# Kernel optimization log

Hardware: AMD Instinct MI355X
Metric: run time of the kernel (lower is better)

## Reference

```python
import jax, jax.numpy as jnp
import numpy as np

N, D, H, DH, FF, NE, NNZ = 4096, 128, 2, 64, 256, 2048, 65536
EPS = 1e-5

def layer_norm(x, g, b):
    m = jnp.mean(x, axis=-1, keepdims=True)
    v = jnp.var(x, axis=-1, keepdims=True)
    return (x - m) / jnp.sqrt(v + EPS) * g + b

def setup_inputs() -> dict:
    key = jax.random.key(0)
    ks = jax.random.split(key, 24)
    s = 0.05
    node_idx = jax.random.randint(ks[1], (NNZ,), 0, N)
    he_idx = jax.random.randint(ks[2], (NNZ,), 0, NE)
    return {
        "x": jax.random.normal(ks[0], (N, D), dtype=jnp.float32),
        "edge": jnp.stack([node_idx, he_idx]).astype(jnp.int64),
        "Wq": jax.random.normal(ks[3], (D, D)) * s, "bq": jnp.zeros((D,)),
        "Wk": jax.random.normal(ks[4], (D, D)) * s, "bk": jnp.zeros((D,)),
        "Wv": jax.random.normal(ks[5], (D, D)) * s, "bv": jnp.zeros((D,)),
        "Wo": jax.random.normal(ks[6], (D, D)) * s, "bo": jnp.zeros((D,)),
        "g_ln1": jnp.ones((D,)), "b_ln1": jnp.zeros((D,)),
        "W1": jax.random.normal(ks[7], (D, FF)) * s, "bf1": jnp.zeros((FF,)),
        "W2": jax.random.normal(ks[8], (FF, D)) * s, "bf2": jnp.zeros((D,)),
        "g_ln2": jnp.ones((D,)), "b_ln2": jnp.zeros((D,)),
        "Wh": jax.random.normal(ks[9], (D, D)) * s, "bh": jnp.zeros((D,)),
    }

def reference(x, edge, Wq, bq, Wk, bk, Wv, bv, Wo, bo, g_ln1, b_ln1,
              W1, bf1, W2, bf2, g_ln2, b_ln2, Wh, bh):
    # dropout layers run in eval mode (identity) for a deterministic reference
    def mha_block(h):
        q = (h @ Wq + bq).reshape(N, H, DH)
        k = (h @ Wk + bk).reshape(N, H, DH)
        v = (h @ Wv + bv).reshape(N, H, DH)
        scores = jnp.einsum('nhd,mhd->hnm', q, k) / jnp.sqrt(jnp.float32(DH))
        attn = jax.nn.softmax(scores, axis=-1)            # [H,N,N]
        o = jnp.einsum('hnm,mhd->nhd', attn, v).reshape(N, D)
        return layer_norm(h + o @ Wo + bo, g_ln1, b_ln1)

    def ff_block(h):
        z = jax.nn.sigmoid(h @ W1 + bf1)
        return layer_norm(h + z @ W2 + bf2, g_ln2, b_ln2)

    h = ff_block(mha_block(x))
    h = ff_block(mha_block(h))

    # HypergraphConv: out = D^{-1} H B^{-1} H^T (X Theta) + bias
    node_idx = edge[0]
    he_idx = edge[1]
    xt = h @ Wh                                            # [N,D]
    ones = jnp.ones((NNZ,), dtype=xt.dtype)
    Bdeg = jax.ops.segment_sum(ones, he_idx, num_segments=NE)
    Binv = jnp.where(Bdeg > 0, 1.0 / Bdeg, 0.0)
    Ddeg = jax.ops.segment_sum(ones, node_idx, num_segments=N)
    Dinv = jnp.where(Ddeg > 0, 1.0 / Ddeg, 0.0)
    e = jax.ops.segment_sum(xt[node_idx], he_idx, num_segments=NE) * Binv[:, None]
    out = jax.ops.segment_sum(e[he_idx], node_idx, num_segments=N) * Dinv[:, None] + bh
    return jax.nn.relu(out)
```

## Files before the change

kernel.cpp:

```cpp
#include <hip/hip_runtime.h>
#include <hip/hip_bf16.h>
#include <cstddef>

#define N_NODES 4096
#define DIM     128
#define NHEAD   2
#define DHEAD   64
#define FFDIM   256
#define NEDGE   2048
#define NNZ_E   65536
#define NSPLIT  8

typedef __attribute__((ext_vector_type(8))) short bf16x8;
typedef __attribute__((ext_vector_type(4))) float f32x4;
typedef unsigned short u16;

__device__ __forceinline__ u16 f2b(float f) {
    unsigned u = __float_as_uint(f);
    return (u16)((u + 0x7FFFu + ((u >> 16) & 1u)) >> 16);
}
__device__ __forceinline__ float b2f_bits(u16 h) {
    return __uint_as_float(((unsigned)h) << 16);
}
__device__ __forceinline__ unsigned cvtpk(float a, float b) {
    unsigned r;
    asm("v_cvt_pk_bf16_f32 %0, %1, %2" : "=v"(r) : "v"(a), "v"(b));
    return r;
}

__global__ void prep(const float* __restrict__ x, float* __restrict__ h,
                     u16* __restrict__ hh, u16* __restrict__ hl,
                     const float* W0, const float* W1, const float* W2,
                     const float* W3, const float* W4, const float* W5,
                     const float* W6,
                     u16* P0, u16* P1, u16* P2, u16* P3, u16* P4, u16* P5, u16* P6,
                     const int* __restrict__ edge_raw,
                     int* __restrict__ nidx, int* __restrict__ hidx,
                     int* __restrict__ cnt_e, int* __restrict__ cnt_n) {
    const int bx = blockIdx.x;
    if (bx < 512) {
        int i4 = bx * 256 + threadIdx.x;
        float4 f4 = ((const float4*)x)[i4];
        ((float4*)h)[i4] = f4;
        ushort4 hi4, lo4;
        hi4.x = f2b(f4.x); lo4.x = f2b(f4.x - b2f_bits(hi4.x));
        hi4.y = f2b(f4.y); lo4.y = f2b(f4.y - b2f_bits(hi4.y));
        hi4.z = f2b(f4.z); lo4.z = f2b(f4.z - b2f_bits(hi4.z));
        hi4.w = f2b(f4.w); lo4.w = f2b(f4.w - b2f_bits(hi4.w));
        ((ushort4*)hh)[i4] = hi4;
        ((ushort4*)hl)[i4] = lo4;
        return;
    }
    if (bx >= 1408) {
        __shared__ int is64_s;
        if (threadIdx.x < 64) {
            int v = edge_raw[2 * threadIdx.x + 1];
            unsigned long long bal = __ballot(v != 0);
            if (threadIdx.x == 0) is64_s = (bal == 0ull) ? 1 : 0;
        }
        __syncthreads();
        const int is64 = is64_s;
        int i = (bx - 1408) * 256 + threadIdx.x;
        if (i < NNZ_E) {
            int ni = (is64 ? edge_raw[2 * i]             : edge_raw[i])         & (N_NODES - 1);
            int he = (is64 ? edge_raw[2 * NNZ_E + 2 * i] : edge_raw[NNZ_E + i]) & (NEDGE - 1);
            nidx[i] = ni;
            hidx[i] = he;
            atomicAdd(&cnt_n[ni], 1);
            atomicAdd(&cnt_e[he], 1);
        }
        return;
    }
    const int p = bx - 512;
    const int sel = p >> 7;
    const float* W; u16* P; int K, NC;
    switch (sel) {
        case 0: W = W0; P = P0; K = 128; NC = 128; break;
        case 1: W = W1; P = P1; K = 128; NC = 128; break;
        case 2: W = W2; P = P2; K = 128; NC = 128; break;
        case 3: W = W3; P = P3; K = 128; NC = 128; break;
        case 4: W = W4; P = P4; K = 128; NC = 128; break;
        case 5: W = W5; P = P5; K = 128; NC = 256; break;
        default: W = W6; P = P6; K = 256; NC = 128; break;
    }
    int i = (p & 127) * 256 + threadIdx.x;
    if (i < K * NC) {
        int k = i / NC, n = i % NC;
        float f = W[i];
        u16 hb = f2b(f);
        size_t o = ((size_t)(k >> 3) * NC + n) * 8 + (k & 7);
        P[o] = hb;
        P[(size_t)K * NC + o] = f2b(f - b2f_bits(hb));
    }
}

__global__ __launch_bounds__(256) void qkv_mfma(const u16* __restrict__ Ah,
                                                const u16* __restrict__ Al,
                                                const u16* __restrict__ Wq,
                                                const u16* __restrict__ Wk,
                                                const u16* __restrict__ Wv,
                                                const float* __restrict__ bq,
                                                const float* __restrict__ bk,
                                                const float* __restrict__ bv,
                                                u16* __restrict__ qb,
                                                u16* __restrict__ kb,
                                                u16* __restrict__ vtb) {
    const int K = 128, NC = 128;
    const int tid = threadIdx.x, w = tid >> 6, lane = tid & 63;
    const int qi = lane & 15, gi = lane >> 4;
    const int row0 = blockIdx.x * 64 + w * 16;
    const int sel = blockIdx.y >> 2;
    const int col0 = (blockIdx.y & 3) * 32;
    const u16* Wp = (sel == 0) ? Wq : (sel == 1) ? Wk : Wv;
    const float* bias = (sel == 0) ? bq : (sel == 1) ? bk : bv;
    const u16* Wlo = Wp + (size_t)K * NC;

    f32x4 acc[2];
    acc[0] = (f32x4){0.f, 0.f, 0.f, 0.f};
    acc[1] = (f32x4){0.f, 0.f, 0.f, 0.f};

#pragma unroll 4
    for (int kc = 0; kc < K / 32; ++kc) {
        const int k0 = kc * 32;
        const size_t ao = (size_t)(row0 + qi) * K + k0 + gi * 8;
        bf16x8 ah = *(const bf16x8*)(Ah + ao);
        bf16x8 al = *(const bf16x8*)(Al + ao);
#pragma unroll
        for (int c = 0; c < 2; ++c) {
            const size_t wo = ((size_t)(k0 / 8 + gi) * NC + col0 + c * 16 + qi) * 8;
            bf16x8 wh = *(const bf16x8*)(Wp + wo);
            bf16x8 wl = *(const bf16x8*)(Wlo + wo);
            acc[c] = __builtin_amdgcn_mfma_f32_16x16x32_bf16(ah, wh, acc[c], 0, 0, 0);
            acc[c] = __builtin_amdgcn_mfma_f32_16x16x32_bf16(al, wh, acc[c], 0, 0, 0);
            acc[c] = __builtin_amdgcn_mfma_f32_16x16x32_bf16(ah, wl, acc[c], 0, 0, 0);
        }
    }

#pragma unroll
    for (int c = 0; c < 2; ++c) {
        const int col = col0 + c * 16 + qi;
        const int hh = col >> 6, d = col & 63;
        float bv_ = bias[col];
        if (sel < 2) {
            u16* dst = (sel == 0) ? qb : kb;
#pragma unroll
            for (int r = 0; r < 4; ++r) {
                const int grow = row0 + gi * 4 + r;
                dst[((size_t)hh * N_NODES + grow) * 64 + d] = f2b(acc[c][r] + bv_);
            }
        } else {
            const int grow0 = row0 + gi * 4;
            uint2 pw;
            pw.x = cvtpk(acc[c][0] + bv_, acc[c][1] + bv_);
            pw.y = cvtpk(acc[c][2] + bv_, acc[c][3] + bv_);
            *(uint2*)&vtb[((size_t)hh * 64 + d) * N_NODES + grow0] = pw;
        }
    }
}

#define ROWP 72
__global__ __launch_bounds__(512, 4) void attn_mfma(const u16* __restrict__ qb,
                                                    const u16* __restrict__ kb,
                                                    const u16* __restrict__ vtb,
                                                    float* __restrict__ op,
                                                    float* __restrict__ mlm,
                                                    float* __restrict__ mll,
                                                    const int* __restrict__ cnt_e,
                                                    const int* __restrict__ cnt_n,
                                                    int* __restrict__ off_e,
                                                    int* __restrict__ off_n,
                                                    int* __restrict__ cur_e,
                                                    int* __restrict__ cur_n) {
    __shared__ __align__(16) u16 k_s[2][64 * ROWP];
    __shared__ __align__(16) u16 vt_s[2][64 * ROWP];
    __shared__ __align__(16) u16 p_s[8][16 * ROWP];

    if (blockIdx.x >= 32) {
        if (blockIdx.y == 0 && blockIdx.z < 2) {
            int* sbuf = (int*)&k_s[0][0];
            const int he_side = (blockIdx.z == 0);
            const int n = he_side ? NEDGE : N_NODES;
            const int* cnt = he_side ? cnt_e : cnt_n;
            int* off = he_side ? off_e : off_n;
            int* cur = he_side ? cur_e : cur_n;
            for (int i = threadIdx.x; i < n; i += 512) sbuf[i] = cnt[i];
            __syncthreads();
            for (int st = 1; st < n; st <<= 1) {
                int v[8]; int nj = 0;
                for (int i = threadIdx.x; i < n; i += 512) v[nj++] = (i >= st) ? sbuf[i - st] : 0;
                __syncthreads();
                nj = 0;
                for (int i = threadIdx.x; i < n; i += 512) sbuf[i] += v[nj++];
                __syncthreads();
            }
            for (int i = threadIdx.x; i < n; i += 512) { off[i + 1] = sbuf[i]; cur[i] = 0; }
            if (threadIdx.x == 0) off[0] = 0;
        }
        return;
    }

    const int h = blockIdx.y;
    const int s = blockIdx.z;
    const int row0 = blockIdx.x * 128;
    const int tid = threadIdx.x;
    const int w = tid >> 6, lane = tid & 63;
    const int qi = lane & 15, gi = lane >> 4;
    const float CE = 0.18033688011f;
    const float THR = 44.36f;

    const u16* qrow = qb + ((size_t)h * N_NODES + row0 + w * 16 + qi) * 64 + gi * 8;
    bf16x8 qf0 = *(const bf16x8*)qrow;
    bf16x8 qf1 = *(const bf16x8*)(qrow + 32);

    f32x4 oc[4];
#pragma unroll
    for (int i = 0; i < 4; ++i) oc[i] = (f32x4){0.f, 0.f, 0.f, 0.f};
    float m_run = -INFINITY, l_run = 0.f;

    const u16* kbh = kb + (size_t)h * N_NODES * 64;
    const u16* vth = vtb + (size_t)h * 64 * N_NODES;

    const int nt0 = s * (N_NODES / 64 / NSPLIT);
    const int nt1 = nt0 + N_NODES / 64 / NSPLIT;
    const int r = tid >> 3, ss = tid & 7;

    {
        const u16* ksrc = kbh + nt0 * 64 * 64;
        *(uint4*)&k_s[0][r * ROWP + ss * 8]  = *(const uint4*)(ksrc + tid * 8);
        *(uint4*)&vt_s[0][r * ROWP + ss * 8] = *(const uint4*)(vth + (size_t)r * N_NODES + nt0 * 64 + ss * 8);
    }
    __syncthreads();
    int cur = 0;

    for (int kt = nt0; kt < nt1; ++kt) {
        uint4 knx, vnx;
        const bool more = (kt + 1 < nt1);
        if (more) {
            const u16* ksrc = kbh + (kt + 1) * 64 * 64;
            knx = *(const uint4*)(ksrc + tid * 8);
            vnx = *(const uint4*)(vth + (size_t)r * N_NODES + (kt + 1) * 64 + ss * 8);
        }

        f32x4 sc[4];
        __builtin_amdgcn_s_setprio(1);
#pragma unroll
        for (int t = 0; t < 4; ++t) {
            const u16* krow = &k_s[cur][(t * 16 + qi) * ROWP + gi * 8];
            bf16x8 ka0 = *(const bf16x8*)krow;
            bf16x8 ka1 = *(const bf16x8*)(krow + 32);
            f32x4 z = (f32x4){0.f, 0.f, 0.f, 0.f};
            z = __builtin_amdgcn_mfma_f32_16x16x32_bf16(ka0, qf0, z, 0, 0, 0);
            sc[t] = __builtin_amdgcn_mfma_f32_16x16x32_bf16(ka1, qf1, z, 0, 0, 0);
        }
        __builtin_amdgcn_s_setprio(0);

        float smax = -INFINITY;
#pragma unroll
        for (int t = 0; t < 4; ++t)
            smax = fmaxf(smax, fmaxf(fmaxf(sc[t][0], sc[t][1]), fmaxf(sc[t][2], sc[t][3])));
        smax = fmaxf(smax, __shfl_xor(smax, 16));
        smax = fmaxf(smax, __shfl_xor(smax, 32));

        const bool renew = !__all(smax <= m_run + THR);
        float alpha;
        if (renew) {
            float mn = fmaxf(m_run, smax);
            alpha = exp2f((m_run - mn) * CE);
            m_run = mn;
        }
        float nb = m_run * CE;
        float psum = 0.f;
#pragma unroll
        for (int t = 0; t < 4; ++t) {
            float p0 = exp2f(fmaf(sc[t][0], CE, -nb));
            float p1 = exp2f(fmaf(sc[t][1], CE, -nb));
            float p2 = exp2f(fmaf(sc[t][2], CE, -nb));
            float p3 = exp2f(fmaf(sc[t][3], CE, -nb));
            psum += (p0 + p1) + (p2 + p3);
            uint2 pw;
            pw.x = cvtpk(p0, p1);
            pw.y = cvtpk(p2, p3);
            *(uint2*)&p_s[w][qi * ROWP + t * 16 + gi * 4] = pw;
        }
        psum += __shfl_xor(psum, 16);
        psum += __shfl_xor(psum, 32);

        if (renew) {
            float a0 = __shfl(alpha, gi * 4 + 0);
            float a1 = __shfl(alpha, gi * 4 + 1);
            float a2 = __shfl(alpha, gi * 4 + 2);
            float a3 = __shfl(alpha, gi * 4 + 3);
#pragma unroll
            for (int d = 0; d < 4; ++d) {
                oc[d][0] *= a0; oc[d][1] *= a1; oc[d][2] *= a2; oc[d][3] *= a3;
            }
            l_run = l_run * alpha + psum;
        } else {
            l_run += psum;
        }

        const u16* prow = &p_s[w][qi * ROWP];
        bf16x8 pa0 = *(const bf16x8*)(prow + gi * 8);
        bf16x8 pa1 = *(const bf16x8*)(prow + 32 + gi * 8);
        __builtin_amdgcn_s_setprio(1);
#pragma unroll
        for (int d = 0; d < 4; ++d) {
            const u16* vrow = &vt_s[cur][(d * 16 + qi) * ROWP + gi * 8];
            bf16x8 vb0 = *(const bf16x8*)vrow;
            bf16x8 vb1 = *(const bf16x8*)(vrow + 32);
            oc[d] = __builtin_amdgcn_mfma_f32_16x16x32_bf16(pa0, vb0, oc[d], 0, 0, 0);
            oc[d] = __builtin_amdgcn_mfma_f32_16x16x32_bf16(pa1, vb1, oc[d], 0, 0, 0);
        }
        __builtin_amdgcn_s_setprio(0);

        if (more) {
            *(uint4*)&k_s[cur ^ 1][r * ROWP + ss * 8]  = knx;
            *(uint4*)&vt_s[cur ^ 1][r * ROWP + ss * 8] = vnx;
        }
        __syncthreads();
        cur ^= 1;
    }

    float* opd = op + (size_t)s * N_NODES * 128;
#pragma unroll
    for (int d = 0; d < 4; ++d) {
        size_t cb = h * 64 + d * 16 + qi;
        opd[(size_t)(row0 + w * 16 + gi * 4 + 0) * 128 + cb] = oc[d][0];
        opd[(size_t)(row0 + w * 16 + gi * 4 + 1) * 128 + cb] = oc[d][1];
        opd[(size_t)(row0 + w * 16 + gi * 4 + 2) * 128 + cb] = oc[d][2];
        opd[(size_t)(row0 + w * 16 + gi * 4 + 3) * 128 + cb] = oc[d][3];
    }
    if (gi == 0) {
        size_t mi = (size_t)s * NHEAD * N_NODES + (size_t)h * N_NODES + row0 + w * 16 + qi;
        mlm[mi] = m_run;
        mll[mi] = l_run;
    }
}

#define ROWA 136
#define ROWZ 264
#define ROWH 132
template<int DO_QKV>
__global__ __launch_bounds__(512) void mega_layer(
        const float* __restrict__ op, const float* __restrict__ mlm,
        const float* __restrict__ mll,
        const u16* __restrict__ wp_o, const float* __restrict__ bo,
        float* __restrict__ h,
        const float* __restrict__ g1, const float* __restrict__ b1,
        const u16* __restrict__ wp_1, const float* __restrict__ bf1,
        const u16* __restrict__ wp_2, const float* __restrict__ bf2,
        const float* __restrict__ g2, const float* __restrict__ b2,
        const u16* __restrict__ wp_q, const u16* __restrict__ wp_k,
        const u16* __restrict__ wp_v,
        const float* __restrict__ bq, const float* __restrict__ bk,
        const float* __restrict__ bv,
        u16* __restrict__ qb, u16* __restrict__ kb, u16* __restrict__ vtb,
        const u16* __restrict__ wp_h, float* __restrict__ xt,
        const int* __restrict__ nidx, const int* __restrict__ hidx,
        const int* __restrict__ off_e, const int* __restrict__ off_n,
        int* __restrict__ cur_e, int* __restrict__ cur_n,
        int* __restrict__ csr_e, int* __restrict__ csr_n) {
    if (DO_QKV && blockIdx.x >= N_NODES / 16) {
        int i = (blockIdx.x - N_NODES / 16) * 512 + threadIdx.x;
        if (i < NNZ_E) {
            int ni = nidx[i], he = hidx[i];
            int p = atomicAdd(&cur_e[he], 1);
            csr_e[off_e[he] + p] = ni;
            int q = atomicAdd(&cur_n[ni], 1);
            csr_n[off_n[ni] + q] = he;
        }
        return;
    }
    __shared__ __align__(16) u16 zbuf[16 * ROWZ * 2];
    __shared__ __align__(16) u16 hp_hi[16 * ROWA];
    __shared__ __align__(16) u16 hp_lo[16 * ROWA];
    __shared__ float hln[16 * ROWH];
    __shared__ float ws_s[NSPLIT][32];
    __shared__ float Linv_s[32];
    __shared__ float wsum[8][16], wsq[8][16];
    const float CE = 0.18033688011f;
    const int tid = threadIdx.x, w = tid >> 6, lane = tid & 63;
    const int qi = lane & 15, gi = lane >> 4;
    const int row0 = blockIdx.x * 16;
    u16* a_hi = zbuf;
    u16* a_lo = zbuf + 16 * ROWA;
    u16* z_hi = zbuf;
    u16* z_lo = zbuf + 16 * ROWZ;

    if (tid < 32) {
        int r = tid >> 1, hd = tid & 1;
        size_t mb = (size_t)hd * N_NODES + row0 + r;
        float m[NSPLIT], l[NSPLIT], mx = -INFINITY;
#pragma unroll
        for (int s = 0; s < NSPLIT; ++s) {
            m[s] = mlm[mb + (size_t)s * NHEAD * N_NODES];
            l[s] = mll[mb + (size_t)s * NHEAD * N_NODES];
            mx = fmaxf(mx, m[s]);
        }
        float L = 0.f;
#pragma unroll
        for (int s = 0; s < NSPLIT; ++s) {
            float ws = exp2f((m[s] - mx) * CE);
            ws_s[s][tid] = ws;
            L += ws * l[s];
        }
        Linv_s[tid] = 1.f / L;
    }
    __syncthreads();

    for (int e = tid; e < 16 * 128; e += 512) {
        int r = e >> 7, c = e & 127, hd = c >> 6;
        size_t idx = (size_t)(row0 + r) * 128 + c;
        float O = 0.f;
#pragma unroll
        for (int s = 0; s < NSPLIT; ++s)
            O += ws_s[s][r * 2 + hd] * op[(size_t)s * N_NODES * 128 + idx];
        float v = O * Linv_s[r * 2 + hd];
        u16 hi = f2b(v);
        a_hi[r * ROWA + c] = hi;
        a_lo[r * ROWA + c] = f2b(v - b2f_bits(hi));
    }
    __syncthreads();

    {
        const u16* Wlo = wp_o + (size_t)128 * 128;
        f32x4 acc = (f32x4){0.f, 0.f, 0.f, 0.f};
        const int col0 = w * 16;
#pragma unroll
        for (int kc = 0; kc < 4; ++kc) {
            const int k0 = kc * 32;
            bf16x8 ah = *(const bf16x8*)&a_hi[qi * ROWA + k0 + gi * 8];
            bf16x8 al = *(const bf16x8*)&a_lo[qi * ROWA + k0 + gi * 8];
            const size_t wo = ((size_t)(k0 / 8 + gi) * 128 + col0 + qi) * 8;
            bf16x8 wh = *(const bf16x8*)(wp_o + wo);
            bf16x8 wl = *(const bf16x8*)(Wlo + wo);
            acc = __builtin_amdgcn_mfma_f32_16x16x32_bf16(ah, wh, acc, 0, 0, 0);
            acc = __builtin_amdgcn_mfma_f32_16x16x32_bf16(al, wh, acc, 0, 0, 0);
            acc = __builtin_amdgcn_mfma_f32_16x16x32_bf16(ah, wl, acc, 0, 0, 0);
        }
        float y[4], rs[4], rq[4];
        const int col = col0 + qi;
        float bvv = bo[col];
#pragma unroll
        for (int r = 0; r < 4; ++r) {
            float v = acc[r] + bvv + h[(size_t)(row0 + gi * 4 + r) * 128 + col];
            y[r] = v;
            rs[r] = v; rq[r] = v * v;
        }
#pragma unroll
        for (int r = 0; r < 4; ++r)
            for (int msk = 1; msk < 16; msk <<= 1) {
                rs[r] += __shfl_xor(rs[r], msk);
                rq[r] += __shfl_xor(rq[r], msk);
            }
        if (qi == 0) {
#pragma unroll
            for (int r = 0; r < 4; ++r) { wsum[w][gi * 4 + r] = rs[r]; wsq[w][gi * 4 + r] = rq[r]; }
        }
        __syncthreads();
#pragma unroll
        for (int r = 0; r < 4; ++r) {
            const int lr = gi * 4 + r;
            float ts = 0.f, tq = 0.f;
#pragma unroll
            for (int ww = 0; ww < 8; ++ww) { ts += wsum[ww][lr]; tq += wsq[ww][lr]; }
            float mean = ts * (1.f / 128.f);
            float var  = tq * (1.f / 128.f) - mean * mean;
            float rstd = rsqrtf(var + 1e-5f);
            float yn = (y[r] - mean) * rstd * g1[col] + b1[col];
            hln[lr * ROWH + col] = yn;
            u16 hi = f2b(yn);
            hp_hi[lr * ROWA + col] = hi;
            hp_lo[lr * ROWA + col] = f2b(yn - b2f_bits(hi));
        }
    }
    __syncthreads();

    {
        const u16* W1lo = wp_1 + (size_t)128 * 256;
        f32x4 acc1[2];
#pragma unroll
        for (int t = 0; t < 2; ++t) acc1[t] = (f32x4){0.f, 0.f, 0.f, 0.f};
#pragma unroll
        for (int kc = 0; kc < 4; ++kc) {
            const int k0 = kc * 32;
            bf16x8 ah = *(const bf16x8*)&hp_hi[qi * ROWA + k0 + gi * 8];
            bf16x8 al = *(const bf16x8*)&hp_lo[qi * ROWA + k0 + gi * 8];
#pragma unroll
            for (int t = 0; t < 2; ++t) {
                const size_t wo = ((size_t)(k0 / 8 + gi) * 256 + w * 32 + t * 16 + qi) * 8;
                bf16x8 wh = *(const bf16x8*)(wp_1 + wo);
                bf16x8 wl = *(const bf16x8*)(W1lo + wo);
                acc1[t] = __builtin_amdgcn_mfma_f32_16x16x32_bf16(ah, wh, acc1[t], 0, 0, 0);
                acc1[t] = __builtin_amdgcn_mfma_f32_16x16x32_bf16(al, wh, acc1[t], 0, 0, 0);
                acc1[t] = __builtin_amdgcn_mfma_f32_16x16x32_bf16(ah, wl, acc1[t], 0, 0, 0);
            }
        }
        __syncthreads();
#pragma unroll
        for (int t = 0; t < 2; ++t) {
            const int col = w * 32 + t * 16 + qi;
            float bvv = bf1[col];
#pragma unroll
            for (int r = 0; r < 4; ++r) {
                float v = acc1[t][r] + bvv;
                v = 1.f / (1.f + __expf(-v));
                u16 hi = f2b(v);
                const int zr = gi * 4 + r;
                z_hi[zr * ROWZ + col] = hi;
                z_lo[zr * ROWZ + col] = f2b(v - b2f_bits(hi));
            }
        }
    }
    __syncthreads();

    {
        const u16* W2lo = wp_2 + (size_t)256 * 128;
        f32x4 acc = (f32x4){0.f, 0.f, 0.f, 0.f};
        const int col0 = w * 16;
#pragma unroll
        for (int kc = 0; kc < 8; ++kc) {
            const int k0 = kc * 32;
            bf16x8 ah = *(const bf16x8*)&z_hi[qi * ROWZ + k0 + gi * 8];
            bf16x8 al = *(const bf16x8*)&z_lo[qi * ROWZ + k0 + gi * 8];
            const size_t wo = ((size_t)(k0 / 8 + gi) * 128 + col0 + qi) * 8;
            bf16x8 wh = *(const bf16x8*)(wp_2 + wo);
            bf16x8 wl = *(const bf16x8*)(W2lo + wo);
            acc = __builtin_amdgcn_mfma_f32_16x16x32_bf16(ah, wh, acc, 0, 0, 0);
            acc = __builtin_amdgcn_mfma_f32_16x16x32_bf16(al, wh, acc, 0, 0, 0);
            acc = __builtin_amdgcn_mfma_f32_16x16x32_bf16(ah, wl, acc, 0, 0, 0);
        }
        float y[4], rs[4], rq[4];
        const int col = col0 + qi;
        float bvv = bf2[col];
#pragma unroll
        for (int r = 0; r < 4; ++r) {
            float v = acc[r] + bvv + hln[(gi * 4 + r) * ROWH + col];
            y[r] = v;
            rs[r] = v; rq[r] = v * v;
        }
#pragma unroll
        for (int r = 0; r < 4; ++r)
            for (int msk = 1; msk < 16; msk <<= 1) {
                rs[r] += __shfl_xor(rs[r], msk);
                rq[r] += __shfl_xor(rq[r], msk);
            }
        if (qi == 0) {
#pragma unroll
            for (int r = 0; r < 4; ++r) { wsum[w][gi * 4 + r] = rs[r]; wsq[w][gi * 4 + r] = rq[r]; }
        }
        __syncthreads();
#pragma unroll
        for (int r = 0; r < 4; ++r) {
            const int lr = gi * 4 + r;
            float ts = 0.f, tq = 0.f;
#pragma unroll
            for (int ww = 0; ww < 8; ++ww) { ts += wsum[ww][lr]; tq += wsq[ww][lr]; }
            float mean = ts * (1.f / 128.f);
            float var  = tq * (1.f / 128.f) - mean * mean;
            float rstd = rsqrtf(var + 1e-5f);
            float yn = (y[r] - mean) * rstd * g2[col] + b2[col];
            if (DO_QKV) h[(size_t)(row0 + lr) * 128 + col] = yn;
            u16 hi = f2b(yn);
            hp_hi[lr * ROWA + col] = hi;
            hp_lo[lr * ROWA + col] = f2b(yn - b2f_bits(hi));
        }
    }

    if (DO_QKV) {
        __syncthreads();
        const int col0 = w * 16;
#pragma unroll
        for (int sel = 0; sel < 3; ++sel) {
            const u16* Wp = (sel == 0) ? wp_q : (sel == 1) ? wp_k : wp_v;
            const float* bias = (sel == 0) ? bq : (sel == 1) ? bk : bv;
            const u16* Wlo = Wp + (size_t)128 * 128;
            f32x4 acc = (f32x4){0.f, 0.f, 0.f, 0.f};
#pragma unroll
            for (int kc = 0; kc < 4; ++kc) {
                const int k0 = kc * 32;
                bf16x8 ah = *(const bf16x8*)&hp_hi[qi * ROWA + k0 + gi * 8];
                bf16x8 al = *(const bf16x8*)&hp_lo[qi * ROWA + k0 + gi * 8];
                const size_t wo = ((size_t)(k0 / 8 + gi) * 128 + col0 + qi) * 8;
                bf16x8 wh = *(const bf16x8*)(Wp + wo);
                bf16x8 wl = *(const bf16x8*)(Wlo + wo);
                acc = __builtin_amdgcn_mfma_f32_16x16x32_bf16(ah, wh, acc, 0, 0, 0);
                acc = __builtin_amdgcn_mfma_f32_16x16x32_bf16(al, wh, acc, 0, 0, 0);
                acc = __builtin_amdgcn_mfma_f32_16x16x32_bf16(ah, wl, acc, 0, 0, 0);
            }
            const int col = col0 + qi;
            const int hh = col >> 6, d = col & 63;
            float bv_ = bias[col];
            if (sel < 2) {
                u16* dst = (sel == 0) ? qb : kb;
#pragma unroll
                for (int r = 0; r < 4; ++r) {
                    const int grow = row0 + gi * 4 + r;
                    dst[((size_t)hh * N_NODES + grow) * 64 + d] = f2b(acc[r] + bv_);
                }
            } else {
                const int grow0 = row0 + gi * 4;
                uint2 pw;
                pw.x = cvtpk(acc[0] + bv_, acc[1] + bv_);
                pw.y = cvtpk(acc[2] + bv_, acc[3] + bv_);
                *(uint2*)&vtb[((size_t)hh * 64 + d) * N_NODES + grow0] = pw;
            }
        }
    } else {
        __syncthreads();
        const u16* Wlo = wp_h + (size_t)128 * 128;
        f32x4 acc = (f32x4){0.f, 0.f, 0.f, 0.f};
        const int col0 = w * 16;
#pragma unroll
        for (int kc = 0; kc < 4; ++kc) {
            const int k0 = kc * 32;
            bf16x8 ah = *(const bf16x8*)&hp_hi[qi * ROWA + k0 + gi * 8];
            bf16x8 al = *(const bf16x8*)&hp_lo[qi * ROWA + k0 + gi * 8];
            const size_t wo = ((size_t)(k0 / 8 + gi) * 128 + col0 + qi) * 8;
            bf16x8 wh = *(const bf16x8*)(wp_h + wo);
            bf16x8 wl = *(const bf16x8*)(Wlo + wo);
            acc = __builtin_amdgcn_mfma_f32_16x16x32_bf16(ah, wh, acc, 0, 0, 0);
            acc = __builtin_amdgcn_mfma_f32_16x16x32_bf16(al, wh, acc, 0, 0, 0);
            acc = __builtin_amdgcn_mfma_f32_16x16x32_bf16(ah, wl, acc, 0, 0, 0);
        }
        const int col = col0 + qi;
#pragma unroll
        for (int r = 0; r < 4; ++r)
            xt[(size_t)(row0 + gi * 4 + r) * 128 + col] = acc[r];
    }
}

__global__ __launch_bounds__(128) void gather_e(const int* __restrict__ off_e,
                                                const int* __restrict__ csr_e,
                                                const float* __restrict__ xt,
                                                float* __restrict__ e_sc) {
    __shared__ int ms[128];
    const int he = blockIdx.x, d = threadIdx.x;
    const int beg = off_e[he], end = off_e[he + 1];
    float a0 = 0.f, a1 = 0.f, a2 = 0.f, a3 = 0.f;
    for (int c = beg; c < end; c += 128) {
        int nl = min(128, end - c);
        if (d < nl) ms[d] = csr_e[c + d];
        __syncthreads();
        int j = 0;
        for (; j + 3 < nl; j += 4) {
            a0 += xt[(size_t)ms[j]     * 128 + d];
            a1 += xt[(size_t)ms[j + 1] * 128 + d];
            a2 += xt[(size_t)ms[j + 2] * 128 + d];
            a3 += xt[(size_t)ms[j + 3] * 128 + d];
        }
        for (; j < nl; ++j) a0 += xt[(size_t)ms[j] * 128 + d];
        __syncthreads();
    }
    float binv = (end > beg) ? 1.f / (float)(end - beg) : 0.f;
    e_sc[(size_t)he * 128 + d] = ((a0 + a1) + (a2 + a3)) * binv;
}

__global__ __launch_bounds__(128) void gather_n(const int* __restrict__ off_n,
                                                const int* __restrict__ csr_n,
                                                const float* __restrict__ e_sc,
                                                const float* __restrict__ bh,
                                                float* __restrict__ out) {
    __shared__ int ms[128];
    const int nn = blockIdx.x, d = threadIdx.x;
    const int beg = off_n[nn], end = off_n[nn + 1];
    float a0 = 0.f, a1 = 0.f, a2 = 0.f, a3 = 0.f;
    for (int c = beg; c < end; c += 128) {
        int nl = min(128, end - c);
        if (d < nl) ms[d] = csr_n[c + d];
        __syncthreads();
        int j = 0;
        for (; j + 3 < nl; j += 4) {
            a0 += e_sc[(size_t)ms[j]     * 128 + d];
            a1 += e_sc[(size_t)ms[j + 1] * 128 + d];
            a2 += e_sc[(size_t)ms[j + 2] * 128 + d];
            a3 += e_sc[(size_t)ms[j + 3] * 128 + d];
        }
        for (; j < nl; ++j) a0 += e_sc[(size_t)ms[j] * 128 + d];
        __syncthreads();
    }
    float dinv = (end > beg) ? 1.f / (float)(end - beg) : 0.f;
    float v = ((a0 + a1) + (a2 + a3)) * dinv + bh[d];
    out[(size_t)nn * 128 + d] = v > 0.f ? v : 0.f;
}

extern "C" void kernel_launch(void* const* d_in, const int* in_sizes, int n_in,
                              void* d_out, int out_size, void* d_ws, size_t ws_size,
                              hipStream_t stream) {
    (void)in_sizes; (void)n_in; (void)out_size; (void)ws_size;
    const float* x    = (const float*)d_in[0];
    const int*   edge = (const int*)  d_in[1];
    const float* Wq = (const float*)d_in[2];  const float* bq  = (const float*)d_in[3];
    const float* Wk = (const float*)d_in[4];  const float* bk  = (const float*)d_in[5];
    const float* Wv = (const float*)d_in[6];  const float* bv  = (const float*)d_in[7];
    const float* Wo = (const float*)d_in[8];  const float* bo  = (const float*)d_in[9];
    const float* g1 = (const float*)d_in[10]; const float* b1  = (const float*)d_in[11];
    const float* W1 = (const float*)d_in[12]; const float* bf1 = (const float*)d_in[13];
    const float* W2 = (const float*)d_in[14]; const float* bf2 = (const float*)d_in[15];
    const float* g2 = (const float*)d_in[16]; const float* b2  = (const float*)d_in[17];
    const float* Wh = (const float*)d_in[18]; const float* bh  = (const float*)d_in[19];
    float* out = (float*)d_out;

    float* B = (float*)d_ws;
    float* h    = B;
    u16*   h_hi = (u16*)(B + 524288);
    u16*   h_lo = (u16*)(B + 786432);
    u16*   qb   = (u16*)(B + 1048576);
    u16*   kb   = (u16*)(B + 1310720);
    u16*   vtb  = (u16*)(B + 1835008);
    float* op   = B + 2097152;
    float* mlm  = B + 6291456;
    float* mll  = B + 6356992;
    float* xt   = B + 6946816;
    float* e_sc = B + 7471104;
    u16*   wp_q = (u16*)(B + 8519680);
    u16*   wp_k = (u16*)(B + 8536064);
    u16*   wp_v = (u16*)(B + 8552448);
    u16*   wp_o = (u16*)(B + 8568832);
    u16*   wp_h = (u16*)(B + 8585216);
    u16*   wp_1 = (u16*)(B + 8601600);
    u16*   wp_2 = (u16*)(B + 8634368);
    int*   cur_e = (int*)(B + 9328640);
    int*   cur_n = (int*)(B + 9330688);
    int*   off_e = (int*)(B + 9334784);
    int*   off_n = (int*)(B + 9336840);
    int*   csr_e = (int*)(B + 9340944);
    int*   csr_n = (int*)(B + 9406480);
    int*   cnt_e = (int*)(B + 9472016);
    int*   cnt_n = (int*)(B + 9474064);
    int*   nidx  = (int*)(B + 9478160);
    int*   hidx  = (int*)(B + 9543696);

    hipMemsetAsync(cnt_e, 0, (NEDGE + N_NODES) * sizeof(int), stream);

    prep<<<1664, 256, 0, stream>>>(x, h, h_hi, h_lo,
                                   Wq, Wk, Wv, Wo, Wh, W1, W2,
                                   wp_q, wp_k, wp_v, wp_o, wp_h, wp_1, wp_2,
                                   edge, nidx, hidx, cnt_e, cnt_n);

    qkv_mfma<<<dim3(64, 12), 256, 0, stream>>>(h_hi, h_lo, wp_q, wp_k, wp_v,
                                               bq, bk, bv, qb, kb, vtb);
    attn_mfma<<<dim3(33, NHEAD, NSPLIT), 512, 0, stream>>>(qb, kb, vtb, op, mlm, mll,
                                                           cnt_e, cnt_n, off_e, off_n,
                                                           cur_e, cur_n);
    mega_layer<1><<<N_NODES / 16 + 128, 512, 0, stream>>>(op, mlm, mll, wp_o, bo, h, g1, b1,
                                                    wp_1, bf1, wp_2, bf2, g2, b2,
                                                    wp_q, wp_k, wp_v, bq, bk, bv,
                                                    qb, kb, vtb, wp_h, xt,
                                                    nidx, hidx, off_e, off_n,
                                                    cur_e, cur_n, csr_e, csr_n);
    attn_mfma<<<dim3(32, NHEAD, NSPLIT), 512, 0, stream>>>(qb, kb, vtb, op, mlm, mll,
                                                           cnt_e, cnt_n, off_e, off_n,
                                                           cur_e, cur_n);
    mega_layer<0><<<N_NODES / 16, 512, 0, stream>>>(op, mlm, mll, wp_o, bo, h, g1, b1,
                                                    wp_1, bf1, wp_2, bf2, g2, b2,
                                                    nullptr, nullptr, nullptr,
                                                    nullptr, nullptr, nullptr,
                                                    nullptr, nullptr, nullptr,
                                                    wp_h, xt,
                                                    nullptr, nullptr, nullptr, nullptr,
                                                    nullptr, nullptr, nullptr, nullptr);

    gather_e<<<NEDGE, 128, 0, stream>>>(off_e, csr_e, xt, e_sc);
    gather_n<<<N_NODES, 128, 0, stream>>>(off_n, csr_n, e_sc, bh, out);
}
```

Before: 218.6 us.

## Vectorize weight packing and combine, split MFMA accumulator chains

Weight packing in prep now has each thread convert eight consecutive-k values and write packed bf16 hi/lo pairs with 16-byte stores. This shrinks the prep grid from 1664 to 840 blocks. The split-softmax combine in mega_layer now uses float4 loads and vectorized hi/lo conversion instead of scalar per-element loops. Every small GEMM (qkv, Wo, W1, W2, Wh) now uses two independent accumulators per output tile, which halves MFMA dependency-chain length at the cost of extra registers and a final add.

```diff
diff --git a/kernel.cpp b/kernel.cpp
--- a/kernel.cpp
+++ b/kernel.cpp
@@ -51,7 +51,7 @@
         ((ushort4*)hl)[i4] = lo4;
         return;
     }
-    if (bx >= 1408) {
+    if (bx >= 584) {
         __shared__ int is64_s;
         if (threadIdx.x < 64) {
             int v = edge_raw[2 * threadIdx.x + 1];
@@ -60,7 +60,7 @@
         }
         __syncthreads();
         const int is64 = is64_s;
-        int i = (bx - 1408) * 256 + threadIdx.x;
+        int i = (bx - 584) * 256 + threadIdx.x;
         if (i < NNZ_E) {
             int ni = (is64 ? edge_raw[2 * i]             : edge_raw[i])         & (N_NODES - 1);
             int he = (is64 ? edge_raw[2 * NNZ_E + 2 * i] : edge_raw[NNZ_E + i]) & (NEDGE - 1);
@@ -72,26 +72,39 @@
         return;
     }
     const int p = bx - 512;
-    const int sel = p >> 7;
-    const float* W; u16* P; int K, NC;
-    switch (sel) {
-        case 0: W = W0; P = P0; K = 128; NC = 128; break;
-        case 1: W = W1; P = P1; K = 128; NC = 128; break;
-        case 2: W = W2; P = P2; K = 128; NC = 128; break;
-        case 3: W = W3; P = P3; K = 128; NC = 128; break;
-        case 4: W = W4; P = P4; K = 128; NC = 128; break;
-        case 5: W = W5; P = P5; K = 128; NC = 256; break;
-        default: W = W6; P = P6; K = 256; NC = 128; break;
-    }
-    int i = (p & 127) * 256 + threadIdx.x;
-    if (i < K * NC) {
-        int k = i / NC, n = i % NC;
-        float f = W[i];
-        u16 hb = f2b(f);
-        size_t o = ((size_t)(k >> 3) * NC + n) * 8 + (k & 7);
-        P[o] = hb;
-        P[(size_t)K * NC + o] = f2b(f - b2f_bits(hb));
-    }
+    int mid, blk0;
+    if (p < 40)      { mid = p >> 3; blk0 = p & 7;  }
+    else if (p < 56) { mid = 5;      blk0 = p - 40; }
+    else             { mid = 6;      blk0 = p - 56; }
+    const float* W; u16* P; int nsh, knc;
+    switch (mid) {
+        case 0: W = W0; P = P0; nsh = 7; knc = 16384; break;
+        case 1: W = W1; P = P1; nsh = 7; knc = 16384; break;
+        case 2: W = W2; P = P2; nsh = 7; knc = 16384; break;
+        case 3: W = W3; P = P3; nsh = 7; knc = 16384; break;
+        case 4: W = W4; P = P4; nsh = 7; knc = 16384; break;
+        case 5: W = W5; P = P5; nsh = 8; knc = 32768; break;
+        default: W = W6; P = P6; nsh = 7; knc = 32768; break;
+    }
+    const int NC = 1 << nsh;
+    int idx = blk0 * 256 + threadIdx.x;
+    int k8 = idx >> nsh, n = idx & (NC - 1);
+    size_t wb = ((size_t)k8 * 8) * NC + n;
+    float f0 = W[wb];          float f1 = W[wb + NC];
+    float f2 = W[wb + 2 * NC]; float f3 = W[wb + 3 * NC];
+    float f4 = W[wb + 4 * NC]; float f5 = W[wb + 5 * NC];
+    float f6 = W[wb + 6 * NC]; float f7 = W[wb + 7 * NC];
+    uint4 hi;
+    hi.x = cvtpk(f0, f1); hi.y = cvtpk(f2, f3);
+    hi.z = cvtpk(f4, f5); hi.w = cvtpk(f6, f7);
+    uint4 lo;
+    lo.x = cvtpk(f0 - __uint_as_float(hi.x << 16), f1 - __uint_as_float(hi.x & 0xFFFF0000u));
+    lo.y = cvtpk(f2 - __uint_as_float(hi.y << 16), f3 - __uint_as_float(hi.y & 0xFFFF0000u));
+    lo.z = cvtpk(f4 - __uint_as_float(hi.z << 16), f5 - __uint_as_float(hi.z & 0xFFFF0000u));
+    lo.w = cvtpk(f6 - __uint_as_float(hi.w << 16), f7 - __uint_as_float(hi.w & 0xFFFF0000u));
+    size_t o = ((size_t)k8 * NC + n) * 8;
+    *(uint4*)&P[o]       = hi;
+    *(uint4*)&P[knc + o] = lo;
 }
 
 __global__ __launch_bounds__(256) void qkv_mfma(const u16* __restrict__ Ah,
@@ -115,11 +128,14 @@
     const float* bias = (sel == 0) ? bq : (sel == 1) ? bk : bv;
     const u16* Wlo = Wp + (size_t)K * NC;
 
-    f32x4 acc[2];
-    acc[0] = (f32x4){0.f, 0.f, 0.f, 0.f};
-    acc[1] = (f32x4){0.f, 0.f, 0.f, 0.f};
-
-#pragma unroll 4
+    f32x4 aca[2], acb[2];
+#pragma unroll
+    for (int c = 0; c < 2; ++c) {
+        aca[c] = (f32x4){0.f, 0.f, 0.f, 0.f};
+        acb[c] = (f32x4){0.f, 0.f, 0.f, 0.f};
+    }
+
+#pragma unroll
     for (int kc = 0; kc < K / 32; ++kc) {
         const int k0 = kc * 32;
         const size_t ao = (size_t)(row0 + qi) * K + k0 + gi * 8;
@@ -127,17 +143,19 @@
         bf16x8 al = *(const bf16x8*)(Al + ao);
 #pragma unroll
         for (int c = 0; c < 2; ++c) {
+            f32x4& acc = (kc < 2) ? aca[c] : acb[c];
             const size_t wo = ((size_t)(k0 / 8 + gi) * NC + col0 + c * 16 + qi) * 8;
             bf16x8 wh = *(const bf16x8*)(Wp + wo);
             bf16x8 wl = *(const bf16x8*)(Wlo + wo);
-            acc[c] = __builtin_amdgcn_mfma_f32_16x16x32_bf16(ah, wh, acc[c], 0, 0, 0);
-            acc[c] = __builtin_amdgcn_mfma_f32_16x16x32_bf16(al, wh, acc[c], 0, 0, 0);
-            acc[c] = __builtin_amdgcn_mfma_f32_16x16x32_bf16(ah, wl, acc[c], 0, 0, 0);
+            acc = __builtin_amdgcn_mfma_f32_16x16x32_bf16(ah, wh, acc, 0, 0, 0);
+            acc = __builtin_amdgcn_mfma_f32_16x16x32_bf16(al, wh, acc, 0, 0, 0);
+            acc = __builtin_amdgcn_mfma_f32_16x16x32_bf16(ah, wl, acc, 0, 0, 0);
         }
     }
 
 #pragma unroll
     for (int c = 0; c < 2; ++c) {
+        f32x4 acc = aca[c] + acb[c];
         const int col = col0 + c * 16 + qi;
         const int hh = col >> 6, d = col & 63;
         float bv_ = bias[col];
@@ -146,13 +164,13 @@
 #pragma unroll
             for (int r = 0; r < 4; ++r) {
                 const int grow = row0 + gi * 4 + r;
-                dst[((size_t)hh * N_NODES + grow) * 64 + d] = f2b(acc[c][r] + bv_);
+                dst[((size_t)hh * N_NODES + grow) * 64 + d] = f2b(acc[r] + bv_);
             }
         } else {
             const int grow0 = row0 + gi * 4;
             uint2 pw;
-            pw.x = cvtpk(acc[c][0] + bv_, acc[c][1] + bv_);
-            pw.y = cvtpk(acc[c][2] + bv_, acc[c][3] + bv_);
+            pw.x = cvtpk(acc[0] + bv_, acc[1] + bv_);
+            pw.y = cvtpk(acc[2] + bv_, acc[3] + bv_);
             *(uint2*)&vtb[((size_t)hh * 64 + d) * N_NODES + grow0] = pw;
         }
     }
@@ -408,27 +426,39 @@
     }
     __syncthreads();
 
-    for (int e = tid; e < 16 * 128; e += 512) {
-        int r = e >> 7, c = e & 127, hd = c >> 6;
-        size_t idx = (size_t)(row0 + r) * 128 + c;
-        float O = 0.f;
-#pragma unroll
-        for (int s = 0; s < NSPLIT; ++s)
-            O += ws_s[s][r * 2 + hd] * op[(size_t)s * N_NODES * 128 + idx];
-        float v = O * Linv_s[r * 2 + hd];
-        u16 hi = f2b(v);
-        a_hi[r * ROWA + c] = hi;
-        a_lo[r * ROWA + c] = f2b(v - b2f_bits(hi));
+    {
+        int r = tid >> 5, c4 = tid & 31;
+        int hd = c4 >> 4;
+        float4 O = {0.f, 0.f, 0.f, 0.f};
+        const float4* opr = (const float4*)(op + (size_t)(row0 + r) * 128) + c4;
+#pragma unroll
+        for (int s = 0; s < NSPLIT; ++s) {
+            float ws = ws_s[s][r * 2 + hd];
+            float4 v = opr[(size_t)s * N_NODES * 32];
+            O.x += ws * v.x; O.y += ws * v.y; O.z += ws * v.z; O.w += ws * v.w;
+        }
+        float li = Linv_s[r * 2 + hd];
+        O.x *= li; O.y *= li; O.z *= li; O.w *= li;
+        uint2 hi, lo;
+        hi.x = cvtpk(O.x, O.y); hi.y = cvtpk(O.z, O.w);
+        lo.x = cvtpk(O.x - __uint_as_float(hi.x << 16),
+                     O.y - __uint_as_float(hi.x & 0xFFFF0000u));
+        lo.y = cvtpk(O.z - __uint_as_float(hi.y << 16),
+                     O.w - __uint_as_float(hi.y & 0xFFFF0000u));
+        *(uint2*)&a_hi[r * ROWA + c4 * 4] = hi;
+        *(uint2*)&a_lo[r * ROWA + c4 * 4] = lo;
     }
     __syncthreads();
 
     {
         const u16* Wlo = wp_o + (size_t)128 * 128;
-        f32x4 acc = (f32x4){0.f, 0.f, 0.f, 0.f};
+        f32x4 ac0 = (f32x4){0.f, 0.f, 0.f, 0.f};
+        f32x4 ac1 = (f32x4){0.f, 0.f, 0.f, 0.f};
         const int col0 = w * 16;
 #pragma unroll
         for (int kc = 0; kc < 4; ++kc) {
             const int k0 = kc * 32;
+            f32x4& acc = (kc < 2) ? ac0 : ac1;
             bf16x8 ah = *(const bf16x8*)&a_hi[qi * ROWA + k0 + gi * 8];
             bf16x8 al = *(const bf16x8*)&a_lo[qi * ROWA + k0 + gi * 8];
             const size_t wo = ((size_t)(k0 / 8 + gi) * 128 + col0 + qi) * 8;
@@ -438,6 +468,7 @@
             acc = __builtin_amdgcn_mfma_f32_16x16x32_bf16(al, wh, acc, 0, 0, 0);
             acc = __builtin_amdgcn_mfma_f32_16x16x32_bf16(ah, wl, acc, 0, 0, 0);
         }
+        f32x4 acc = ac0 + ac1;
         float y[4], rs[4], rq[4];
         const int col = col0 + qi;
         float bvv = bo[col];
@@ -478,9 +509,12 @@
 
     {
         const u16* W1lo = wp_1 + (size_t)128 * 256;
-        f32x4 acc1[2];
-#pragma unroll
-        for (int t = 0; t < 2; ++t) acc1[t] = (f32x4){0.f, 0.f, 0.f, 0.f};
+        f32x4 acc1[2][2];
+#pragma unroll
+        for (int t = 0; t < 2; ++t) {
+            acc1[t][0] = (f32x4){0.f, 0.f, 0.f, 0.f};
+            acc1[t][1] = (f32x4){0.f, 0.f, 0.f, 0.f};
+        }
 #pragma unroll
         for (int kc = 0; kc < 4; ++kc) {
             const int k0 = kc * 32;
@@ -488,22 +522,24 @@
             bf16x8 al = *(const bf16x8*)&hp_lo[qi * ROWA + k0 + gi * 8];
 #pragma unroll
             for (int t = 0; t < 2; ++t) {
+                f32x4& acc = acc1[t][kc < 2 ? 0 : 1];
                 const size_t wo = ((size_t)(k0 / 8 + gi) * 256 + w * 32 + t * 16 + qi) * 8;
                 bf16x8 wh = *(const bf16x8*)(wp_1 + wo);
                 bf16x8 wl = *(const bf16x8*)(W1lo + wo);
-                acc1[t] = __builtin_amdgcn_mfma_f32_16x16x32_bf16(ah, wh, acc1[t], 0, 0, 0);
-                acc1[t] = __builtin_amdgcn_mfma_f32_16x16x32_bf16(al, wh, acc1[t], 0, 0, 0);
-                acc1[t] = __builtin_amdgcn_mfma_f32_16x16x32_bf16(ah, wl, acc1[t], 0, 0, 0);
+                acc = __builtin_amdgcn_mfma_f32_16x16x32_bf16(ah, wh, acc, 0, 0, 0);
+                acc = __builtin_amdgcn_mfma_f32_16x16x32_bf16(al, wh, acc, 0, 0, 0);
+                acc = __builtin_amdgcn_mfma_f32_16x16x32_bf16(ah, wl, acc, 0, 0, 0);
             }
         }
         __syncthreads();
 #pragma unroll
         for (int t = 0; t < 2; ++t) {
+            f32x4 acc = acc1[t][0] + acc1[t][1];
             const int col = w * 32 + t * 16 + qi;
             float bvv = bf1[col];
 #pragma unroll
             for (int r = 0; r < 4; ++r) {
-                float v = acc1[t][r] + bvv;
+                float v = acc[r] + bvv;
                 v = 1.f / (1.f + __expf(-v));
                 u16 hi = f2b(v);
                 const int zr = gi * 4 + r;
@@ -516,11 +552,13 @@
 
     {
         const u16* W2lo = wp_2 + (size_t)256 * 128;
-        f32x4 acc = (f32x4){0.f, 0.f, 0.f, 0.f};
+        f32x4 ac0 = (f32x4){0.f, 0.f, 0.f, 0.f};
+        f32x4 ac1 = (f32x4){0.f, 0.f, 0.f, 0.f};
         const int col0 = w * 16;
 #pragma unroll
         for (int kc = 0; kc < 8; ++kc) {
             const int k0 = kc * 32;
+            f32x4& acc = (kc < 4) ? ac0 : ac1;
             bf16x8 ah = *(const bf16x8*)&z_hi[qi * ROWZ + k0 + gi * 8];
             bf16x8 al = *(const bf16x8*)&z_lo[qi * ROWZ + k0 + gi * 8];
             const size_t wo = ((size_t)(k0 / 8 + gi) * 128 + col0 + qi) * 8;
@@ -530,6 +568,7 @@
             acc = __builtin_amdgcn_mfma_f32_16x16x32_bf16(al, wh, acc, 0, 0, 0);
             acc = __builtin_amdgcn_mfma_f32_16x16x32_bf16(ah, wl, acc, 0, 0, 0);
         }
+        f32x4 acc = ac0 + ac1;
         float y[4], rs[4], rq[4];
         const int col = col0 + qi;
         float bvv = bf2[col];
@@ -575,10 +614,12 @@
             const u16* Wp = (sel == 0) ? wp_q : (sel == 1) ? wp_k : wp_v;
             const float* bias = (sel == 0) ? bq : (sel == 1) ? bk : bv;
             const u16* Wlo = Wp + (size_t)128 * 128;
-            f32x4 acc = (f32x4){0.f, 0.f, 0.f, 0.f};
+            f32x4 ac0 = (f32x4){0.f, 0.f, 0.f, 0.f};
+            f32x4 ac1 = (f32x4){0.f, 0.f, 0.f, 0.f};
 #pragma unroll
             for (int kc = 0; kc < 4; ++kc) {
                 const int k0 = kc * 32;
+                f32x4& acc = (kc < 2) ? ac0 : ac1;
                 bf16x8 ah = *(const bf16x8*)&hp_hi[qi * ROWA + k0 + gi * 8];
                 bf16x8 al = *(const bf16x8*)&hp_lo[qi * ROWA + k0 + gi * 8];
                 const size_t wo = ((size_t)(k0 / 8 + gi) * 128 + col0 + qi) * 8;
@@ -588,6 +629,7 @@
                 acc = __builtin_amdgcn_mfma_f32_16x16x32_bf16(al, wh, acc, 0, 0, 0);
                 acc = __builtin_amdgcn_mfma_f32_16x16x32_bf16(ah, wl, acc, 0, 0, 0);
             }
+            f32x4 acc = ac0 + ac1;
             const int col = col0 + qi;
             const int hh = col >> 6, d = col & 63;
             float bv_ = bias[col];
@@ -609,11 +651,13 @@
     } else {
         __syncthreads();
         const u16* Wlo = wp_h + (size_t)128 * 128;
-        f32x4 acc = (f32x4){0.f, 0.f, 0.f, 0.f};
+        f32x4 ac0 = (f32x4){0.f, 0.f, 0.f, 0.f};
+        f32x4 ac1 = (f32x4){0.f, 0.f, 0.f, 0.f};
         const int col0 = w * 16;
 #pragma unroll
         for (int kc = 0; kc < 4; ++kc) {
             const int k0 = kc * 32;
+            f32x4& acc = (kc < 2) ? ac0 : ac1;
             bf16x8 ah = *(const bf16x8*)&hp_hi[qi * ROWA + k0 + gi * 8];
             bf16x8 al = *(const bf16x8*)&hp_lo[qi * ROWA + k0 + gi * 8];
             const size_t wo = ((size_t)(k0 / 8 + gi) * 128 + col0 + qi) * 8;
@@ -623,6 +667,7 @@
             acc = __builtin_amdgcn_mfma_f32_16x16x32_bf16(al, wh, acc, 0, 0, 0);
             acc = __builtin_amdgcn_mfma_f32_16x16x32_bf16(ah, wl, acc, 0, 0, 0);
         }
+        f32x4 acc = ac0 + ac1;
         const int col = col0 + qi;
 #pragma unroll
         for (int r = 0; r < 4; ++r)
@@ -733,10 +778,10 @@
 
     hipMemsetAsync(cnt_e, 0, (NEDGE + N_NODES) * sizeof(int), stream);
 
-    prep<<<1664, 256, 0, stream>>>(x, h, h_hi, h_lo,
-                                   Wq, Wk, Wv, Wo, Wh, W1, W2,
-                                   wp_q, wp_k, wp_v, wp_o, wp_h, wp_1, wp_2,
-                                   edge, nidx, hidx, cnt_e, cnt_n);
+    prep<<<840, 256, 0, stream>>>(x, h, h_hi, h_lo,
+                                  Wq, Wk, Wv, Wo, Wh, W1, W2,
+                                  wp_q, wp_k, wp_v, wp_o, wp_h, wp_1, wp_2,
+                                  edge, nidx, hidx, cnt_e, cnt_n);
 
     qkv_mfma<<<dim3(64, 12), 256, 0, stream>>>(h_hi, h_lo, wp_q, wp_k, wp_v,
                                                bq, bk, bv, qb, kb, vtb);
```

Result: no change. 219.0 us (+0.2%).
